# Kernel optimization log

Measured on AMD Instinct MI355X. Metric: run time of the kernel, lower is better.

## Reference

```python
import jax, jax.numpy as jnp
import numpy as np
import math

HIDDEN = 2048
NUM_HEADS = 16
HEAD_DIM = 128
ROPE_BASE = 10000.0


def _rope_emb(seq_len, dim, dtype):
    # freqs[i, j] = i * base**(-2j/dim); emb = concat(freqs, freqs) -> [S, dim]
    inv_freq = 1.0 / (ROPE_BASE ** (jnp.arange(0, dim, 2, dtype=jnp.float32) / dim))
    t = jnp.arange(seq_len, dtype=jnp.float32)
    freqs = t[:, None] * inv_freq[None, :]            # [S, dim/2]
    return jnp.concatenate([freqs, freqs], axis=-1).astype(dtype)  # [S, dim]


def _apply_rope(x, emb):
    # x: [B, H, S, D]; emb: [S, D] broadcast over batch and heads.
    # Roll-based rotary variant from the source: x*cos + roll(x, 1, -1)*sin
    e = emb[None, None, :, :]
    return x * jnp.cos(e) + jnp.roll(x, shift=1, axis=-1) * jnp.sin(e)


def setup_inputs() -> dict:
    key = jax.random.key(0)
    ks = jax.random.split(key, 5)
    B, S = 2, 2048
    scale = 1.0 / math.sqrt(HIDDEN)
    return {
        "hidden_states": jax.random.normal(ks[0], (B, S, HIDDEN), dtype=jnp.float32),
        "Wq": jax.random.normal(ks[1], (HIDDEN, HIDDEN), dtype=jnp.float32) * scale,
        "Wk": jax.random.normal(ks[2], (HIDDEN, HIDDEN), dtype=jnp.float32) * scale,
        "Wv": jax.random.normal(ks[3], (HIDDEN, HIDDEN), dtype=jnp.float32) * scale,
        "Wo": jax.random.normal(ks[4], (HIDDEN, HIDDEN), dtype=jnp.float32) * scale,
    }


def reference(hidden_states, Wq, Wk, Wv, Wo):
    B, S, _ = hidden_states.shape
    H, D = NUM_HEADS, HEAD_DIM

    def split_heads(x):
        return x.reshape(B, S, H, D).transpose(0, 2, 1, 3)  # [B,H,S,D]

    q = split_heads(hidden_states @ Wq)
    k = split_heads(hidden_states @ Wk)
    v = split_heads(hidden_states @ Wv)

    emb = _rope_emb(S, D, hidden_states.dtype)  # [S, D]
    q = _apply_rope(q, emb)
    k = _apply_rope(k, emb)

    scores = jnp.einsum("bhqd,bhkd->bhqk", q, k) / math.sqrt(D)  # [B,H,S,S]
    probs = jax.nn.softmax(scores, axis=-1)
    ctx = jnp.einsum("bhqk,bhkd->bhqd", probs, v)  # [B,H,S,D]
    ctx = ctx.transpose(0, 2, 1, 3).reshape(B, S, H * D)
    return ctx @ Wo
```

## Files before the change

kernel.cpp:

```cpp
#include <hip/hip_runtime.h>

#define HIDDEN 2048
#define SEQ    2048
#define BATCH  2
#define NHEAD  16
#define HDIM   128

typedef __attribute__((ext_vector_type(4))) int    i32x4;
typedef __attribute__((ext_vector_type(4))) float  f32x4;
typedef __attribute__((ext_vector_type(8))) __bf16 bf16x8;

__device__ __forceinline__ unsigned short f2bf(float f) {
    return __builtin_bit_cast(unsigned short, (__bf16)f);
}
__device__ __forceinline__ float bf2f(unsigned short h) {
    unsigned u = ((unsigned)h) << 16;
    return __builtin_bit_cast(float, u);
}
__device__ __forceinline__ void gl_lds16(const unsigned short* g, unsigned short* l) {
    __builtin_amdgcn_global_load_lds(
        (const __attribute__((address_space(1))) unsigned int*)g,
        (__attribute__((address_space(3))) unsigned int*)l, 16, 0, 0);
}

__global__ void k_rope_tables(float* __restrict__ ctab, float* __restrict__ stab) {
    int idx = blockIdx.x * 256 + threadIdx.x;
    int t = idx >> 6, i = idx & 63;
    float inv = expf(-(float)i * 0.14391156831212793f);
    float ang = (float)t * inv;
    ctab[idx] = cosf(ang);
    stab[idx] = sinf(ang);
}

__global__ void k_cvt_bf16(const float* __restrict__ in, unsigned short* __restrict__ out, int n4) {
    int idx = blockIdx.x * blockDim.x + threadIdx.x;
    if (idx < n4) {
        float4 v = ((const float4*)in)[idx];
        ushort4 o;
        o.x = f2bf(v.x); o.y = f2bf(v.y); o.z = f2bf(v.z); o.w = f2bf(v.w);
        ((ushort4*)out)[idx] = o;
    }
}

__global__ void k_transcvt4(const float* __restrict__ W0, const float* __restrict__ W1,
                            const float* __restrict__ W2, const float* __restrict__ W3,
                            unsigned short* __restrict__ O0, unsigned short* __restrict__ O1,
                            unsigned short* __restrict__ O2, unsigned short* __restrict__ O3) {
    __shared__ float tile[32][33];
    int z = blockIdx.z;
    const float* in = (z == 0) ? W0 : (z == 1) ? W1 : (z == 2) ? W2 : W3;
    unsigned short* out = (z == 0) ? O0 : (z == 1) ? O1 : (z == 2) ? O2 : O3;
    float scl = (z == 0) ? 0.12751743f : 1.0f;
    int tx = threadIdx.x, ty = threadIdx.y;
    int x = blockIdx.x * 32 + tx, y0 = blockIdx.y * 32;
#pragma unroll
    for (int i = 0; i < 4; i++)
        tile[ty + i * 8][tx] = in[(size_t)(y0 + ty + i * 8) * HIDDEN + x];
    __syncthreads();
    int x2 = blockIdx.y * 32 + tx, y2 = blockIdx.x * 32;
#pragma unroll
    for (int i = 0; i < 4; i++)
        out[(size_t)(y2 + ty + i * 8) * HIDDEN + x2] = f2bf(tile[tx][ty + i * 8] * scl);
}

template <int OUTB>
__global__ __launch_bounds__(512, 1) void k_gemm256(
    const unsigned short* __restrict__ A,
    const unsigned short* __restrict__ B0, const unsigned short* __restrict__ B1,
    const unsigned short* __restrict__ B2,
    void* __restrict__ C0, void* __restrict__ C1, void* __restrict__ C2,
    int K)
{
    __shared__ __align__(16) unsigned short S[3 * 24576];
    const int nwg = gridDim.x;
    int id = blockIdx.x;
    int wg = (id & 7) * (nwg >> 3) + (id >> 3);
    const int z = wg >> 8;
    const int my = (wg >> 4) & 15, nx = wg & 15;
    const unsigned short* Bm = (z == 0) ? B0 : (z == 1 ? B1 : B2);
    void* Cv = (z == 0) ? C0 : (z == 1 ? C1 : C2);
    const int m0 = my * 256, n0 = nx * 128;
    const int tid = threadIdx.x, l = tid & 63, w = tid >> 6;
    const int wm = w >> 1, wn = w & 1;
    const int lr = l & 15, lg = l >> 4;

    const unsigned short* sg[6];
    int so[6];
#pragma unroll
    for (int j = 0; j < 4; j++) {
        int c = tid + j * 512, row = c >> 3, k8 = c & 7;
        sg[j] = A + (size_t)(m0 + row) * K + ((k8 ^ (row & 7)) * 8);
        so[j] = row * 64 + k8 * 8;
    }
#pragma unroll
    for (int j = 0; j < 2; j++) {
        int c = tid + j * 512, row = c >> 3, k8 = c & 7;
        sg[4 + j] = Bm + (size_t)(n0 + row) * K + ((k8 ^ (row & 7)) * 8);
        so[4 + j] = 16384 + row * 64 + k8 * 8;
    }

    f32x4 acc[4][4] = {};

    auto stage = [&](int t) {
        unsigned short* buf = &S[(t % 3) * 24576];
        const int ko = t * 64;
#pragma unroll
        for (int j = 0; j < 6; j++) gl_lds16(sg[j] + ko, &buf[so[j]]);
    };
    auto compute = [&](int t) {
        const unsigned short* buf = &S[(t % 3) * 24576];
        const unsigned short* bb = buf + 16384;
        const int xk0 = (lg ^ (lr & 7)) * 8, xk1 = ((4 + lg) ^ (lr & 7)) * 8;
        i32x4 af0[4], af1[4], bf0[4], bf1[4];
#pragma unroll
        for (int i = 0; i < 4; i++) {
            int R = (wm * 64 + i * 16 + lr) * 64;
            af0[i] = *(const i32x4*)&buf[R + xk0];
            af1[i] = *(const i32x4*)&buf[R + xk1];
        }
#pragma unroll
        for (int j = 0; j < 4; j++) {
            int R = (wn * 64 + j * 16 + lr) * 64;
            bf0[j] = *(const i32x4*)&bb[R + xk0];
            bf1[j] = *(const i32x4*)&bb[R + xk1];
        }
        __builtin_amdgcn_s_setprio(1);
#pragma unroll
        for (int i = 0; i < 4; i++)
#pragma unroll
            for (int j = 0; j < 4; j++)
                acc[i][j] = __builtin_amdgcn_mfma_f32_16x16x32_bf16(
                    __builtin_bit_cast(bf16x8, af0[i]),
                    __builtin_bit_cast(bf16x8, bf0[j]), acc[i][j], 0, 0, 0);
#pragma unroll
        for (int i = 0; i < 4; i++)
#pragma unroll
            for (int j = 0; j < 4; j++)
                acc[i][j] = __builtin_amdgcn_mfma_f32_16x16x32_bf16(
                    __builtin_bit_cast(bf16x8, af1[i]),
                    __builtin_bit_cast(bf16x8, bf1[j]), acc[i][j], 0, 0, 0);
        __builtin_amdgcn_s_setprio(0);
    };

    const int nt = K / 64;
    stage(0); stage(1);
    for (int t = 0; t < nt - 1; ++t) {
        asm volatile("s_waitcnt vmcnt(6)" ::: "memory");
        __builtin_amdgcn_s_barrier();
        __builtin_amdgcn_sched_barrier(0);
        if (t < nt - 2) stage(t + 2);
        compute(t);
    }
    asm volatile("s_waitcnt vmcnt(0)" ::: "memory");
    __builtin_amdgcn_s_barrier();
    __builtin_amdgcn_sched_barrier(0);
    compute(nt - 1);

    if (OUTB && z == 2) {
        unsigned short* Vt = (unsigned short*)Cv;
        const int bb_ = m0 >> 11;
        const int tb = (m0 & 2047) + wm * 64;
#pragma unroll
        for (int i = 0; i < 4; i++)
#pragma unroll
            for (int j = 0; j < 4; j++) {
                int t0 = tb + i * 16 + lg * 4;
                int n = n0 + wn * 64 + j * 16 + lr;
                ushort4 pk;
                pk.x = f2bf(acc[i][j][0]); pk.y = f2bf(acc[i][j][1]);
                pk.z = f2bf(acc[i][j][2]); pk.w = f2bf(acc[i][j][3]);
                *(ushort4*)&Vt[((size_t)(bb_ * 2048 + n)) * 2048 + t0] = pk;
            }
    } else {
#pragma unroll
        for (int i = 0; i < 4; i++)
#pragma unroll
            for (int j = 0; j < 4; j++)
#pragma unroll
                for (int r = 0; r < 4; r++) {
                    int m = m0 + wm * 64 + i * 16 + lg * 4 + r;
                    int n = n0 + wn * 64 + j * 16 + lr;
                    float v = acc[i][j][r];
                    if (OUTB) ((unsigned short*)Cv)[(size_t)m * 2048 + n] = f2bf(v);
                    else      ((float*)Cv)[(size_t)m * 2048 + n] = v;
                }
    }
}

__global__ void k_rope(unsigned short* __restrict__ Q, unsigned short* __restrict__ Kb,
                       const float* __restrict__ ctab, const float* __restrict__ stab)
{
    const int tid = threadIdx.x, l = tid & 63, w = tid >> 6;
    int hr = blockIdx.x * 4 + w;
    unsigned short* X = blockIdx.y ? Kb : Q;
    int bt = hr >> 4, h = hr & 15, t = bt & (SEQ - 1);
    size_t base = (size_t)bt * HIDDEN + h * HDIM;
    int d0 = l * 2;
    ushort2 xv = *(const ushort2*)&X[base + d0];
    float x0 = bf2f(xv.x), x1 = bf2f(xv.y);
    float prev = __shfl(x1, (l + 63) & 63);
    int i0 = d0 & 63, i1 = (d0 + 1) & 63;
    float c0 = ctab[t * 64 + i0], s0 = stab[t * 64 + i0];
    float c1 = ctab[t * 64 + i1], s1 = stab[t * 64 + i1];
    ushort2 ov;
    ov.x = f2bf(x0 * c0 + prev * s0);
    ov.y = f2bf(x1 * c1 + x0 * s1);
    *(ushort2*)&X[base + d0] = ov;
}

__global__ __launch_bounds__(512) void k_attn(
    const unsigned short* __restrict__ Q, const unsigned short* __restrict__ K,
    const unsigned short* __restrict__ Vt, unsigned short* __restrict__ ctx)
{
    __shared__ __align__(16) unsigned short Klds[2][64 * 128];
    __shared__ __align__(16) unsigned short Vlds[2][128 * 64];
    __shared__ __align__(16) unsigned short Plds[8][32 * 64];
    const int tid = threadIdx.x, l = tid & 63, w = tid >> 6;
    const int lr = l & 15, lg = l >> 4;
    const int bid = blockIdx.x;
    const int sX = bid >> 3;
    const int bh = (bid & 7) * 4 + (sX >> 3);
    const int q0 = (sX & 7) * 256;
    const int b = bh >> 4, h = bh & 15;

    i32x4 qf[2][4];
#pragma unroll
    for (int qh = 0; qh < 2; qh++) {
        const unsigned short* qbase =
            Q + (size_t)(b * SEQ + q0 + w * 32 + qh * 16 + lr) * HIDDEN + h * HDIM + lg * 8;
#pragma unroll
        for (int c = 0; c < 4; c++) qf[qh][c] = *(const i32x4*)(qbase + c * 32);
    }

    const unsigned short* kg[2];
    const unsigned short* vg[2];
    int kl[2], vl[2];
#pragma unroll
    for (int c = 0; c < 2; c++) {
        int cc = tid + c * 512;
        {   int row = cc >> 4, ch = cc & 15, sch = ch ^ (row & 7);
            kg[c] = K + (size_t)(b * SEQ + row) * HIDDEN + h * HDIM + sch * 8;
            kl[c] = cc * 8; }
        {   int row = cc >> 3, ch = cc & 7, sch = ch ^ (row & 7);
            vg[c] = Vt + (size_t)(bh * HDIM + row) * SEQ + sch * 8;
            vl[c] = cc * 8; }
    }

    auto stage = [&](int t, int bsel) {
        const size_t ko = (size_t)t * 64;
#pragma unroll
        for (int c = 0; c < 2; c++) {
            gl_lds16(kg[c] + ko * HIDDEN, &Klds[bsel][kl[c]]);
            gl_lds16(vg[c] + ko,          &Vlds[bsel][vl[c]]);
        }
    };

    f32x4 acc[2][8] = {};
    float m_run[2] = {-1e30f, -1e30f}, l_run[2] = {0.f, 0.f};

    stage(0, 0);
    const int nt = SEQ / 64;
    for (int t = 0; t < nt; ++t) {
        asm volatile("s_waitcnt vmcnt(0)" ::: "memory");
        __builtin_amdgcn_s_barrier();
        asm volatile("" ::: "memory");
        __builtin_amdgcn_sched_barrier(0);
        if (t + 1 < nt) stage(t + 1, (t + 1) & 1);
        const unsigned short* Kb_ = Klds[t & 1];
        const unsigned short* Vb_ = Vlds[t & 1];

        f32x4 s[4][2];
        __builtin_amdgcn_s_setprio(1);
#pragma unroll
        for (int ks = 0; ks < 4; ks++) {
            s[ks][0] = f32x4{0.f, 0.f, 0.f, 0.f};
            s[ks][1] = f32x4{0.f, 0.f, 0.f, 0.f};
#pragma unroll
            for (int c = 0; c < 4; c++) {
                i32x4 kf = *(const i32x4*)&Kb_[(ks * 16 + lr) * 128 + ((c * 4 + lg) ^ (lr & 7)) * 8];
                s[ks][0] = __builtin_amdgcn_mfma_f32_16x16x32_bf16(
                    __builtin_bit_cast(bf16x8, kf), __builtin_bit_cast(bf16x8, qf[0][c]),
                    s[ks][0], 0, 0, 0);
                s[ks][1] = __builtin_amdgcn_mfma_f32_16x16x32_bf16(
                    __builtin_bit_cast(bf16x8, kf), __builtin_bit_cast(bf16x8, qf[1][c]),
                    s[ks][1], 0, 0, 0);
            }
        }
        __builtin_amdgcn_s_setprio(0);

        float p[2][4][4];
        float fac[2];
        bool need_any = false;
#pragma unroll
        for (int qh = 0; qh < 2; qh++) {
            float mx0 = fmaxf(fmaxf(s[0][qh][0], s[0][qh][1]), fmaxf(s[0][qh][2], s[0][qh][3]));
            float mx1 = fmaxf(fmaxf(s[1][qh][0], s[1][qh][1]), fmaxf(s[1][qh][2], s[1][qh][3]));
            float mx2 = fmaxf(fmaxf(s[2][qh][0], s[2][qh][1]), fmaxf(s[2][qh][2], s[2][qh][3]));
            float mx3 = fmaxf(fmaxf(s[3][qh][0], s[3][qh][1]), fmaxf(s[3][qh][2], s[3][qh][3]));
            float pmax = fmaxf(fmaxf(mx0, mx1), fmaxf(mx2, mx3));
            pmax = fmaxf(pmax, __shfl_xor(pmax, 16));
            pmax = fmaxf(pmax, __shfl_xor(pmax, 32));
            bool need = pmax > m_run[qh] + 8.0f;
            fac[qh] = need ? __builtin_amdgcn_exp2f(m_run[qh] - pmax) : 1.0f;
            float mn = need ? pmax : m_run[qh];
            m_run[qh] = mn;
            float psum = 0.f;
#pragma unroll
            for (int ks = 0; ks < 4; ks++) {
                float e0 = __builtin_amdgcn_exp2f(s[ks][qh][0] - mn);
                float e1 = __builtin_amdgcn_exp2f(s[ks][qh][1] - mn);
                float e2 = __builtin_amdgcn_exp2f(s[ks][qh][2] - mn);
                float e3 = __builtin_amdgcn_exp2f(s[ks][qh][3] - mn);
                p[qh][ks][0] = e0; p[qh][ks][1] = e1;
                p[qh][ks][2] = e2; p[qh][ks][3] = e3;
                psum += (e0 + e1) + (e2 + e3);
            }
            psum += __shfl_xor(psum, 16);
            psum += __shfl_xor(psum, 32);
            l_run[qh] = l_run[qh] * fac[qh] + psum;
            need_any |= need;
        }

        unsigned short* pw = &Plds[w][0];
#pragma unroll
        for (int qh = 0; qh < 2; qh++)
#pragma unroll
            for (int ks = 0; ks < 4; ks++) {
                ushort4 pk;
                pk.x = f2bf(p[qh][ks][0]); pk.y = f2bf(p[qh][ks][1]);
                pk.z = f2bf(p[qh][ks][2]); pk.w = f2bf(p[qh][ks][3]);
                int chunk = ks * 2 + (lg >> 1);
                *(ushort4*)&pw[(qh * 16 + lr) * 64 + ((chunk ^ (lr & 7)) * 8) + (lg & 1) * 4] = pk;
            }

        if (__any((int)need_any)) {
#pragma unroll
            for (int qh = 0; qh < 2; qh++) {
                float facq[4];
#pragma unroll
                for (int r = 0; r < 4; r++) facq[r] = __shfl(fac[qh], lg * 4 + r);
#pragma unroll
                for (int db = 0; db < 8; db++)
#pragma unroll
                    for (int r = 0; r < 4; r++) acc[qh][db][r] *= facq[r];
            }
        }

        __builtin_amdgcn_s_setprio(1);
#pragma unroll
        for (int kk = 0; kk < 2; kk++) {
            i32x4 pf0 = *(const i32x4*)&pw[(lr) * 64 + ((kk * 4 + lg) ^ (lr & 7)) * 8];
            i32x4 pf1 = *(const i32x4*)&pw[(16 + lr) * 64 + ((kk * 4 + lg) ^ (lr & 7)) * 8];
#pragma unroll
            for (int db = 0; db < 8; db++) {
                i32x4 vf = *(const i32x4*)&Vb_[(db * 16 + lr) * 64 + ((kk * 4 + lg) ^ (lr & 7)) * 8];
                acc[0][db] = __builtin_amdgcn_mfma_f32_16x16x32_bf16(
                    __builtin_bit_cast(bf16x8, pf0), __builtin_bit_cast(bf16x8, vf),
                    acc[0][db], 0, 0, 0);
                acc[1][db] = __builtin_amdgcn_mfma_f32_16x16x32_bf16(
                    __builtin_bit_cast(bf16x8, pf1), __builtin_bit_cast(bf16x8, vf),
                    acc[1][db], 0, 0, 0);
            }
        }
        __builtin_amdgcn_s_setprio(0);
    }

#pragma unroll
    for (int qh = 0; qh < 2; qh++) {
        float inv[4];
#pragma unroll
        for (int r = 0; r < 4; r++) inv[r] = 1.0f / __shfl(l_run[qh], lg * 4 + r);
#pragma unroll
        for (int db = 0; db < 8; db++)
#pragma unroll
            for (int r = 0; r < 4; r++) {
                int trow = q0 + w * 32 + qh * 16 + lg * 4 + r;
                ctx[(size_t)(b * SEQ + trow) * HIDDEN + h * HDIM + db * 16 + lr] =
                    f2bf(acc[qh][db][r] * inv[r]);
            }
    }
}

extern "C" void kernel_launch(void* const* d_in, const int* in_sizes, int n_in,
                              void* d_out, int out_size, void* d_ws, size_t ws_size,
                              hipStream_t stream)
{
    (void)in_sizes; (void)n_in; (void)out_size; (void)ws_size;
    const float* X  = (const float*)d_in[0];
    const float* Wq = (const float*)d_in[1];
    const float* Wk = (const float*)d_in[2];
    const float* Wv = (const float*)d_in[3];
    const float* Wo = (const float*)d_in[4];
    float* out = (float*)d_out;
    char* ws = (char*)d_ws;

    unsigned short* Xb  = (unsigned short*)(ws);
    unsigned short* WqT = (unsigned short*)(ws + 16777216);
    unsigned short* WkT = (unsigned short*)(ws + 25165824);
    unsigned short* WvT = (unsigned short*)(ws + 33554432);
    unsigned short* WoT = (unsigned short*)(ws + 41943040);
    unsigned short* Qb  = (unsigned short*)(ws + 50331648);
    unsigned short* Kb  = (unsigned short*)(ws + 67108864);
    unsigned short* Vt  = (unsigned short*)(ws + 100663296);
    unsigned short* Cx  = (unsigned short*)(ws + 117440512);
    float* ctab = (float*)(ws + 134217728);
    float* stab = (float*)(ws + 134742016);

    k_rope_tables<<<512, 256, 0, stream>>>(ctab, stab);
    k_cvt_bf16<<<8192, 256, 0, stream>>>(X, Xb, 2097152);
    k_transcvt4<<<dim3(64, 64, 4), dim3(32, 8), 0, stream>>>(Wq, Wk, Wv, Wo,
                                                             WqT, WkT, WvT, WoT);
    k_gemm256<1><<<768, 512, 0, stream>>>(Xb, WqT, WkT, WvT, Qb, Kb, Vt, 2048);
    k_rope<<<dim3(16384, 2), 256, 0, stream>>>(Qb, Kb, ctab, stab);
    k_attn<<<256, 512, 0, stream>>>(Qb, Kb, Vt, Cx);
    k_gemm256<0><<<256, 512, 0, stream>>>(Cx, WoT, WoT, WoT, out, out, out, 2048);
}
```

Baseline: 279.5 us.

## Fuse RoPE into QKV GEMM epilogue and merge table/convert kernels

Applies the roll-based rotary embedding inside the Q/K projection GEMM epilogue, taking the left neighbour via wave shuffles and an LDS exchange across wave column halves. This removes the separate RoPE kernel and its extra read and write of Q and K. The RoPE table build is also merged into the input bf16 conversion kernel, saving one launch. The epilogue now does strided scalar bf16 stores, table loads and an extra barrier, which adds work inside the GEMM. RoPE is also applied before bf16 rounding, so numerics shift slightly.

```diff
diff --git a/kernel.cpp b/kernel.cpp
--- a/kernel.cpp
+++ b/kernel.cpp
@@ -23,22 +23,22 @@
         (__attribute__((address_space(3))) unsigned int*)l, 16, 0, 0);
 }
 
-__global__ void k_rope_tables(float* __restrict__ ctab, float* __restrict__ stab) {
-    int idx = blockIdx.x * 256 + threadIdx.x;
-    int t = idx >> 6, i = idx & 63;
-    float inv = expf(-(float)i * 0.14391156831212793f);
-    float ang = (float)t * inv;
-    ctab[idx] = cosf(ang);
-    stab[idx] = sinf(ang);
-}
-
-__global__ void k_cvt_bf16(const float* __restrict__ in, unsigned short* __restrict__ out, int n4) {
-    int idx = blockIdx.x * blockDim.x + threadIdx.x;
-    if (idx < n4) {
+__global__ void k_cvt_tables(const float* __restrict__ in, unsigned short* __restrict__ out,
+                             float* __restrict__ ctab, float* __restrict__ stab) {
+    int bid = blockIdx.x;
+    if (bid < 8192) {
+        int idx = bid * 256 + threadIdx.x;
         float4 v = ((const float4*)in)[idx];
         ushort4 o;
         o.x = f2bf(v.x); o.y = f2bf(v.y); o.z = f2bf(v.z); o.w = f2bf(v.w);
         ((ushort4*)out)[idx] = o;
+    } else {
+        int idx = (bid - 8192) * 256 + threadIdx.x;
+        int t = idx >> 6, i = idx & 63;
+        float inv = expf(-(float)i * 0.14391156831212793f);
+        float ang = (float)t * inv;
+        ctab[idx] = cosf(ang);
+        stab[idx] = sinf(ang);
     }
 }
 
@@ -69,6 +69,7 @@
     const unsigned short* __restrict__ B0, const unsigned short* __restrict__ B1,
     const unsigned short* __restrict__ B2,
     void* __restrict__ C0, void* __restrict__ C1, void* __restrict__ C2,
+    const float* __restrict__ ctab, const float* __restrict__ stab,
     int K)
 {
     __shared__ __align__(16) unsigned short S[3 * 24576];
@@ -171,6 +172,41 @@
                 pk.z = f2bf(acc[i][j][2]); pk.w = f2bf(acc[i][j][3]);
                 *(ushort4*)&Vt[((size_t)(bb_ * 2048 + n)) * 2048 + t0] = pk;
             }
+    } else if (OUTB) {
+        float* xch = (float*)S;
+        if (lr == 15) {
+#pragma unroll
+            for (int i = 0; i < 4; i++)
+#pragma unroll
+                for (int r = 0; r < 4; r++)
+                    xch[(((wm << 1) | wn) * 4 + i) * 16 + lg * 4 + r] = acc[i][3][r];
+        }
+        __syncthreads();
+        unsigned short* Co = (unsigned short*)Cv;
+#pragma unroll
+        for (int i = 0; i < 4; i++)
+#pragma unroll
+            for (int r = 0; r < 4; r++) {
+                int m = m0 + wm * 64 + i * 16 + lg * 4 + r;
+                int t = m & 2047;
+                float ldsprev = xch[(((wm << 1) | (wn ^ 1)) * 4 + i) * 16 + lg * 4 + r];
+#pragma unroll
+                for (int j = 0; j < 4; j++) {
+                    float v = acc[i][j][r];
+                    float pA = __shfl(v, l - 1);
+                    float prev;
+                    if (j == 0) {
+                        prev = (lr == 0) ? ldsprev : pA;
+                    } else {
+                        float pB = __shfl(acc[i][j - 1][r], (l & 48) + 15);
+                        prev = (lr == 0) ? pB : pA;
+                    }
+                    float cc = ctab[t * 64 + j * 16 + lr];
+                    float ss = stab[t * 64 + j * 16 + lr];
+                    int n = n0 + wn * 64 + j * 16 + lr;
+                    Co[(size_t)m * 2048 + n] = f2bf(v * cc + prev * ss);
+                }
+            }
     } else {
 #pragma unroll
         for (int i = 0; i < 4; i++)
@@ -180,32 +216,9 @@
                 for (int r = 0; r < 4; r++) {
                     int m = m0 + wm * 64 + i * 16 + lg * 4 + r;
                     int n = n0 + wn * 64 + j * 16 + lr;
-                    float v = acc[i][j][r];
-                    if (OUTB) ((unsigned short*)Cv)[(size_t)m * 2048 + n] = f2bf(v);
-                    else      ((float*)Cv)[(size_t)m * 2048 + n] = v;
+                    ((float*)Cv)[(size_t)m * 2048 + n] = acc[i][j][r];
                 }
     }
-}
-
-__global__ void k_rope(unsigned short* __restrict__ Q, unsigned short* __restrict__ Kb,
-                       const float* __restrict__ ctab, const float* __restrict__ stab)
-{
-    const int tid = threadIdx.x, l = tid & 63, w = tid >> 6;
-    int hr = blockIdx.x * 4 + w;
-    unsigned short* X = blockIdx.y ? Kb : Q;
-    int bt = hr >> 4, h = hr & 15, t = bt & (SEQ - 1);
-    size_t base = (size_t)bt * HIDDEN + h * HDIM;
-    int d0 = l * 2;
-    ushort2 xv = *(const ushort2*)&X[base + d0];
-    float x0 = bf2f(xv.x), x1 = bf2f(xv.y);
-    float prev = __shfl(x1, (l + 63) & 63);
-    int i0 = d0 & 63, i1 = (d0 + 1) & 63;
-    float c0 = ctab[t * 64 + i0], s0 = stab[t * 64 + i0];
-    float c1 = ctab[t * 64 + i1], s1 = stab[t * 64 + i1];
-    ushort2 ov;
-    ov.x = f2bf(x0 * c0 + prev * s0);
-    ov.y = f2bf(x1 * c1 + x0 * s1);
-    *(ushort2*)&X[base + d0] = ov;
 }
 
 __global__ __launch_bounds__(512) void k_attn(
@@ -406,12 +419,12 @@
     float* ctab = (float*)(ws + 134217728);
     float* stab = (float*)(ws + 134742016);
 
-    k_rope_tables<<<512, 256, 0, stream>>>(ctab, stab);
-    k_cvt_bf16<<<8192, 256, 0, stream>>>(X, Xb, 2097152);
+    k_cvt_tables<<<8704, 256, 0, stream>>>(X, Xb, ctab, stab);
     k_transcvt4<<<dim3(64, 64, 4), dim3(32, 8), 0, stream>>>(Wq, Wk, Wv, Wo,
                                                              WqT, WkT, WvT, WoT);
-    k_gemm256<1><<<768, 512, 0, stream>>>(Xb, WqT, WkT, WvT, Qb, Kb, Vt, 2048);
-    k_rope<<<dim3(16384, 2), 256, 0, stream>>>(Qb, Kb, ctab, stab);
+    k_gemm256<1><<<768, 512, 0, stream>>>(Xb, WqT, WkT, WvT, Qb, Kb, Vt,
+                                          ctab, stab, 2048);
     k_attn<<<256, 512, 0, stream>>>(Qb, Kb, Vt, Cx);
-    k_gemm256<0><<<256, 512, 0, stream>>>(Cx, WoT, WoT, WoT, out, out, out, 2048);
-}
+    k_gemm256<0><<<256, 512, 0, stream>>>(Cx, WoT, WoT, WoT, out, out, out,
+                                          nullptr, nullptr, 2048);
+}
```

Result: faster. 261.4 us (-6.5%).
